# Kernel tuning notes

Measured on AMD Instinct MI355X. Metric: run time of the kernel, lower is better.

## Reference

```python
import jax, jax.numpy as jnp
import numpy as np

N, E, G = 20000, 320000, 32


def setup_inputs() -> dict:
    key = jax.random.key(0)
    ks = list(jax.random.split(key, 16))
    def nrm(i, shape, s):
        return jax.random.normal(ks[i], shape, jnp.float32) * s
    inp = {}
    inp['x'] = nrm(0, (N, 768), 1.0)
    inp['edge_index'] = jax.random.randint(ks[1], (2, E), 0, N)
    inp['batch'] = jnp.sort(jax.random.randint(ks[2], (N,), 0, G))
    # xavier-ish scales
    inp['proj_w'] = nrm(3, (768, 768), 0.036); inp['proj_b'] = jnp.zeros((768,), jnp.float32)
    inp['gat1_w'] = nrm(4, (768, 1024), 0.033)
    inp['att1_src'] = nrm(5, (4, 256), 0.06); inp['att1_dst'] = nrm(6, (4, 256), 0.06)
    inp['gat1_b'] = jnp.zeros((1024,), jnp.float32)
    inp['ln1_g'] = jnp.ones((1024,), jnp.float32); inp['ln1_b'] = jnp.zeros((1024,), jnp.float32)
    inp['gat2_w'] = nrm(7, (1024, 1024), 0.031)
    inp['att2_src'] = nrm(8, (4, 256), 0.06); inp['att2_dst'] = nrm(9, (4, 256), 0.06)
    inp['gat2_b'] = jnp.zeros((1024,), jnp.float32)
    inp['ln2_g'] = jnp.ones((1024,), jnp.float32); inp['ln2_b'] = jnp.zeros((1024,), jnp.float32)
    inp['gat3_w'] = nrm(10, (1024, 256), 0.04)
    inp['att3_src'] = nrm(11, (1, 256), 0.08); inp['att3_dst'] = nrm(12, (1, 256), 0.08)
    inp['gat3_b'] = jnp.zeros((256,), jnp.float32)
    inp['ln3_g'] = jnp.ones((256,), jnp.float32); inp['ln3_b'] = jnp.zeros((256,), jnp.float32)
    inp['cls1_w'] = nrm(13, (768, 128), 0.047); inp['cls1_b'] = jnp.zeros((128,), jnp.float32)
    inp['cls2_w'] = nrm(14, (128, 1), 0.12); inp['cls2_b'] = jnp.zeros((1,), jnp.float32)
    return inp


def layer_norm(x, g, b, eps=1e-5):
    mu = x.mean(-1, keepdims=True)
    v = ((x - mu) ** 2).mean(-1, keepdims=True)
    return (x - mu) * jax.lax.rsqrt(v + eps) * g + b


def gat_conv(x, src, dst, W, a_src, a_dst, bias, concat):
    # PyG GATConv (eval mode): linear -> per-head additive attention ->
    # segment softmax over incoming edges of each dst node -> scatter-sum.
    n = x.shape[0]
    H, C = a_src.shape
    h = (x @ W).reshape(n, H, C)                      # [N,H,C]
    e_s = (h * a_src[None]).sum(-1)                   # [N,H]
    e_d = (h * a_dst[None]).sum(-1)                   # [N,H]
    logits = jax.nn.leaky_relu(e_s[src] + e_d[dst], 0.2)   # [Etot,H]
    m = jax.ops.segment_max(logits, dst, num_segments=n)   # self-loops -> no empty segments
    ex = jnp.exp(logits - m[dst])
    den = jax.ops.segment_sum(ex, dst, num_segments=n)
    alpha = ex / (den[dst] + 1e-16)                   # [Etot,H]
    out = jax.ops.segment_sum(h[src] * alpha[:, :, None], dst, num_segments=n)  # [N,H,C]
    out = out.reshape(n, H * C) if concat else out.mean(axis=1)
    return out + bias


def reference(x, edge_index, batch, proj_w, proj_b,
              gat1_w, att1_src, att1_dst, gat1_b, ln1_g, ln1_b,
              gat2_w, att2_src, att2_dst, gat2_b, ln2_g, ln2_b,
              gat3_w, att3_src, att3_dst, gat3_b, ln3_g, ln3_b,
              cls1_w, cls1_b, cls2_w, cls2_b):
    n = x.shape[0]
    loop = jnp.arange(n)
    src = jnp.concatenate([edge_index[0], loop])  # GATConv adds self-loops
    dst = jnp.concatenate([edge_index[1], loop])
    h = jax.nn.elu(x @ proj_w + proj_b)
    x1 = jax.nn.elu(layer_norm(gat_conv(h, src, dst, gat1_w, att1_src, att1_dst, gat1_b, True), ln1_g, ln1_b))
    x2 = jax.nn.elu(layer_norm(gat_conv(x1, src, dst, gat2_w, att2_src, att2_dst, gat2_b, True), ln2_g, ln2_b)) + x1
    x3 = jax.nn.elu(layer_norm(gat_conv(x2, src, dst, gat3_w, att3_src, att3_dst, gat3_b, False), ln3_g, ln3_b))
    cnt = jax.ops.segment_sum(jnp.ones((n, 1), x3.dtype), batch, num_segments=G)
    s = jax.ops.segment_sum(x3, batch, num_segments=G)
    mean = s / jnp.maximum(cnt, 1.0)
    mx = jax.ops.segment_max(x3, batch, num_segments=G)
    pooled = jnp.concatenate([mean, mx, s], axis=1)   # [G, 3*256]
    out = jax.nn.relu(pooled @ cls1_w + cls1_b) @ cls2_w + cls2_b
    return out.reshape(-1)
```

## Files before the change

kernel.cpp:

```cpp
#include <hip/hip_runtime.h>
#include <math.h>

typedef float floatx4 __attribute__((ext_vector_type(4)));
typedef _Float16 f16x8 __attribute__((ext_vector_type(8)));
typedef _Float16 f16x4 __attribute__((ext_vector_type(4)));

__device__ __forceinline__ unsigned encf(float f) {
    unsigned u = __float_as_uint(f);
    return (u & 0x80000000u) ? ~u : (u | 0x80000000u);
}
__device__ __forceinline__ float decf(unsigned u) {
    u = (u & 0x80000000u) ? (u & 0x7FFFFFFFu) : ~u;
    return __uint_as_float(u);
}
__device__ __forceinline__ void glds16(const void* g, void* l) {
    __builtin_amdgcn_global_load_lds(
        (const __attribute__((address_space(1))) unsigned int*)g,
        (__attribute__((address_space(3))) unsigned int*)l, 16, 0, 0);
}

__global__ __launch_bounds__(256) void cvt_f16_kernel(
    const float* __restrict__ in, _Float16* __restrict__ out, size_t n4)
{
    size_t i = (size_t)blockIdx.x * 256 + threadIdx.x;
    if (i >= n4) return;
    float4 v = ((const float4*)in)[i];
    f16x4 o;
    o[0] = (_Float16)v.x; o[1] = (_Float16)v.y; o[2] = (_Float16)v.z; o[3] = (_Float16)v.w;
    ((f16x4*)out)[i] = o;
}

__global__ __launch_bounds__(256) void wt_kernel(
    const float* __restrict__ w, _Float16* __restrict__ wt, int K, int N)
{
    __shared__ float t[32][33];
    int bx = blockIdx.x * 32, by = blockIdx.y * 32;
    int tx = threadIdx.x & 31, ty = threadIdx.x >> 5;
    for (int r = ty; r < 32; r += 8)
        t[r][tx] = w[(size_t)(by + r) * N + bx + tx];
    __syncthreads();
    for (int r = ty; r < 32; r += 8)
        wt[(size_t)(bx + r) * K + by + tx] = (_Float16)t[tx][r];
}

__global__ __launch_bounds__(256) void gemm_f16(
    const _Float16* __restrict__ A, const _Float16* __restrict__ BT,
    const float* __restrict__ bias, _Float16* __restrict__ C,
    int M, int K, int N, int act)
{
    __shared__ _Float16 Al[2][128 * 32];
    __shared__ _Float16 Bl[2][128 * 32];
    int tid = threadIdx.x;
    int lane = tid & 63, wave = tid >> 6;
    int row0 = blockIdx.y * 128, col0 = blockIdx.x * 128;
    int wm = (wave >> 1) * 64, wn = (wave & 1) * 64;
    int l15 = lane & 15, quad = lane >> 4;

    int rg0 = wave * 2, rg1 = rg0 + 1;
    int srow0 = rg0 * 16 + (lane >> 2);
    int srow1 = rg1 * 16 + (lane >> 2);
    int scol = (lane & 3) * 8;
    int arow0 = row0 + srow0; if (arow0 > M - 1) arow0 = M - 1;
    int arow1 = row0 + srow1; if (arow1 > M - 1) arow1 = M - 1;
    const _Float16* gA0 = A + (size_t)arow0 * K + scol;
    const _Float16* gA1 = A + (size_t)arow1 * K + scol;
    const _Float16* gB0 = BT + (size_t)(col0 + srow0) * K + scol;
    const _Float16* gB1 = BT + (size_t)(col0 + srow1) * K + scol;

    floatx4 acc[4][4] = {};

    glds16(gA0, &Al[0][rg0 * 512]);
    glds16(gA1, &Al[0][rg1 * 512]);
    glds16(gB0, &Bl[0][rg0 * 512]);
    glds16(gB1, &Bl[0][rg1 * 512]);

    int nk = K >> 5;
    for (int it = 0; it < nk; it++) {
        int cur = it & 1, nxt = cur ^ 1;
        __syncthreads();
        if (it + 1 < nk) {
            int k1 = (it + 1) << 5;
            glds16(gA0 + k1, &Al[nxt][rg0 * 512]);
            glds16(gA1 + k1, &Al[nxt][rg1 * 512]);
            glds16(gB0 + k1, &Bl[nxt][rg0 * 512]);
            glds16(gB1 + k1, &Bl[nxt][rg1 * 512]);
        }
        f16x8 af[4], bfr[4];
        #pragma unroll
        for (int i = 0; i < 4; i++) {
            af[i]  = *(const f16x8*)&Al[cur][(wm + i * 16 + l15) * 32 + quad * 8];
            bfr[i] = *(const f16x8*)&Bl[cur][(wn + i * 16 + l15) * 32 + quad * 8];
        }
        #pragma unroll
        for (int i = 0; i < 4; i++)
            #pragma unroll
            for (int j = 0; j < 4; j++)
                acc[i][j] = __builtin_amdgcn_mfma_f32_16x16x32_f16(af[i], bfr[j], acc[i][j], 0, 0, 0);
    }

    #pragma unroll
    for (int i = 0; i < 4; i++) {
        #pragma unroll
        for (int v = 0; v < 4; v++) {
            int gr = row0 + wm + i * 16 + quad * 4 + v;
            if (gr >= M) continue;
            #pragma unroll
            for (int j = 0; j < 4; j++) {
                int gc = col0 + wn + j * 16 + l15;
                float val = acc[i][j][v];
                if (bias) val += bias[gc];
                if (act) val = val > 0.f ? val : (expf(val) - 1.f);
                C[(size_t)gr * N + gc] = (_Float16)val;
            }
        }
    }
}

__global__ __launch_bounds__(256) void attn_scores_kernel(
    const _Float16* __restrict__ h, const float* __restrict__ asrc, const float* __restrict__ adst,
    float* __restrict__ es, float* __restrict__ ed, int Nn, int H)
{
    int wid = (blockIdx.x * 256 + threadIdx.x) >> 6;
    int lane = threadIdx.x & 63;
    if (wid >= Nn * H) return;
    int node = wid / H, hh = wid % H;
    const _Float16* hp = h + (size_t)node * H * 256 + hh * 256 + lane * 4;
    f16x4 v = *(const f16x4*)hp;
    float ss = 0.f, sd = 0.f;
    #pragma unroll
    for (int j = 0; j < 4; j++) {
        float f = (float)v[j];
        ss = fmaf(f, asrc[hh * 256 + lane * 4 + j], ss);
        sd = fmaf(f, adst[hh * 256 + lane * 4 + j], sd);
    }
    #pragma unroll
    for (int o = 32; o; o >>= 1) { ss += __shfl_down(ss, o); sd += __shfl_down(sd, o); }
    if (lane == 0) { es[wid] = ss; ed[wid] = sd; }
}

__global__ __launch_bounds__(256) void csr_init(int* __restrict__ deg, int Nn) {
    int i = blockIdx.x * 256 + threadIdx.x;
    if (i < Nn) deg[i] = 1;
}
__global__ __launch_bounds__(256) void csr_count(const int* __restrict__ ei, int* __restrict__ deg, int E) {
    int i = blockIdx.x * 256 + threadIdx.x;
    if (i < E) atomicAdd(&deg[ei[E + i]], 1);
}
__global__ __launch_bounds__(256) void scan1(const int* __restrict__ deg, int* __restrict__ incl,
                                             int* __restrict__ bsums, int Nn) {
    __shared__ int sd[256];
    int idx = blockIdx.x * 256 + threadIdx.x;
    sd[threadIdx.x] = (idx < Nn) ? deg[idx] : 0;
    __syncthreads();
    for (int o = 1; o < 256; o <<= 1) {
        int x = (threadIdx.x >= (unsigned)o) ? sd[threadIdx.x - o] : 0;
        __syncthreads();
        sd[threadIdx.x] += x;
        __syncthreads();
    }
    if (idx < Nn) incl[idx] = sd[threadIdx.x];
    if (threadIdx.x == 255) bsums[blockIdx.x] = sd[255];
}
__global__ void scan2(int* __restrict__ bsums, int nb) {
    if (blockIdx.x == 0 && threadIdx.x == 0) {
        int run = 0;
        for (int i = 0; i < nb; i++) { int v = bsums[i]; bsums[i] = run; run += v; }
    }
}
__global__ __launch_bounds__(256) void scan3(const int* __restrict__ incl, const int* __restrict__ deg,
                                             const int* __restrict__ bsums, int* __restrict__ rowstart,
                                             int* __restrict__ cursor, int Nn) {
    int idx = blockIdx.x * 256 + threadIdx.x;
    if (idx >= Nn) return;
    int rs = incl[idx] - deg[idx] + bsums[blockIdx.x];
    rowstart[idx] = rs;
    cursor[idx] = rs;
}
__global__ __launch_bounds__(256) void csr_fill(const int* __restrict__ ei, int* __restrict__ cursor,
                                                int* __restrict__ csrc, int* __restrict__ cdst,
                                                int E, int Nn) {
    int i = blockIdx.x * 256 + threadIdx.x;
    if (i >= E + Nn) return;
    int s, d;
    if (i < E) { s = ei[i]; d = ei[E + i]; } else { s = d = i - E; }
    int pos = atomicAdd(&cursor[d], 1);
    csrc[pos] = s;
    cdst[pos] = d;
}

template<int H>
__global__ __launch_bounds__(256) void seg_mz(
    const int* __restrict__ rowstart, const int* __restrict__ deg,
    const int* __restrict__ csrc, const float* __restrict__ es,
    const float* __restrict__ ed, float2* __restrict__ mz, int Nn)
{
    int d = (blockIdx.x * 256 + threadIdx.x) >> 6;
    int lane = threadIdx.x & 63;
    if (d >= Nn) return;
    constexpr int S = 64 / H;
    int head = lane & (H - 1);
    int slot = lane / H;
    int st = rowstart[d], dg = deg[d];
    float edv = ed[d * H + head];
    float m = -1e30f;
    for (int j = slot; j < dg; j += S) {
        float l = es[csrc[st + j] * H + head] + edv;
        l = l > 0.f ? l : 0.2f * l;
        m = fmaxf(m, l);
    }
    #pragma unroll
    for (int o = H; o < 64; o <<= 1) m = fmaxf(m, __shfl_xor(m, o));
    float z = 0.f;
    for (int j = slot; j < dg; j += S) {
        float l = es[csrc[st + j] * H + head] + edv;
        l = l > 0.f ? l : 0.2f * l;
        z += expf(l - m);
    }
    #pragma unroll
    for (int o = H; o < 64; o <<= 1) z += __shfl_xor(z, o);
    if (lane < H) mz[d * H + lane] = make_float2(m, 1.f / (z + 1e-16f));
}

template<int H>
__global__ __launch_bounds__(256) void edge_alpha(
    const int* __restrict__ csrc, const int* __restrict__ cdst,
    const float* __restrict__ es, const float* __restrict__ ed,
    const float2* __restrict__ mz, float* __restrict__ wse, int Etot)
{
    int i = blockIdx.x * 256 + threadIdx.x;
    if (i >= Etot) return;
    int s = csrc[i], d = cdst[i];
    float a[H];
    #pragma unroll
    for (int hh = 0; hh < H; hh++) {
        float l = es[s * H + hh] + ed[d * H + hh];
        l = l > 0.f ? l : 0.2f * l;
        float2 mzv = mz[d * H + hh];
        a[hh] = expf(l - mzv.x) * mzv.y;
    }
    if constexpr (H == 4) {
        ((float4*)wse)[i] = make_float4(a[0], a[1], a[2], a[3]);
    } else {
        wse[i] = a[0];
    }
}

template<int H>
__global__ __launch_bounds__(64 * H) void gat_gather_ln(
    const int* __restrict__ rowstart, const int* __restrict__ deg,
    const int* __restrict__ csrc, const float* __restrict__ wse,
    const _Float16* __restrict__ h,
    const float* __restrict__ bias, const float* __restrict__ gam,
    const float* __restrict__ bet, const float* resid,
    float* xout, _Float16* xout16)
{
    constexpr int T = 64 * H;
    constexpr int NW = H;
    const int HC = T * 4;
    int d = blockIdx.x;
    int t = threadIdx.x;
    int lane = t & 63, wave = t >> 6;
    int head2 = t >> 6;
    int st = rowstart[d], dg = deg[d];
    const _Float16* hb = h + (size_t)t * 4;

    float a0 = 0.f, a1 = 0.f, a2 = 0.f, a3 = 0.f;
    int j = 0;
    for (; j + 2 <= dg; j += 2) {
        int s0 = csrc[st + j], s1 = csrc[st + j + 1];
        float w0 = wse[(size_t)(st + j) * H + head2];
        float w1 = wse[(size_t)(st + j + 1) * H + head2];
        f16x4 v0 = *(const f16x4*)(hb + (size_t)s0 * HC);
        f16x4 v1 = *(const f16x4*)(hb + (size_t)s1 * HC);
        a0 += w0 * (float)v0[0] + w1 * (float)v1[0];
        a1 += w0 * (float)v0[1] + w1 * (float)v1[1];
        a2 += w0 * (float)v0[2] + w1 * (float)v1[2];
        a3 += w0 * (float)v0[3] + w1 * (float)v1[3];
    }
    if (j < dg) {
        int s0 = csrc[st + j];
        float w0 = wse[(size_t)(st + j) * H + head2];
        f16x4 v0 = *(const f16x4*)(hb + (size_t)s0 * HC);
        a0 += w0 * (float)v0[0];
        a1 += w0 * (float)v0[1];
        a2 += w0 * (float)v0[2];
        a3 += w0 * (float)v0[3];
    }

    int c0 = t * 4;
    a0 += bias[c0]; a1 += bias[c0 + 1]; a2 += bias[c0 + 2]; a3 += bias[c0 + 3];

    __shared__ float sm[NW];
    float sum = a0 + a1 + a2 + a3;
    #pragma unroll
    for (int o = 32; o; o >>= 1) sum += __shfl_down(sum, o);
    if (lane == 0) sm[wave] = sum;
    __syncthreads();
    float tot = 0.f;
    #pragma unroll
    for (int w2 = 0; w2 < NW; w2++) tot += sm[w2];
    float mean = tot / (float)HC;
    float d0 = a0 - mean, d1 = a1 - mean, d2 = a2 - mean, d3 = a3 - mean;
    float sq = d0 * d0 + d1 * d1 + d2 * d2 + d3 * d3;
    #pragma unroll
    for (int o = 32; o; o >>= 1) sq += __shfl_down(sq, o);
    __syncthreads();
    if (lane == 0) sm[wave] = sq;
    __syncthreads();
    tot = 0.f;
    #pragma unroll
    for (int w2 = 0; w2 < NW; w2++) tot += sm[w2];
    float rstd = rsqrtf(tot / (float)HC + 1e-5f);

    float y0 = d0 * rstd * gam[c0]     + bet[c0];
    float y1 = d1 * rstd * gam[c0 + 1] + bet[c0 + 1];
    float y2 = d2 * rstd * gam[c0 + 2] + bet[c0 + 2];
    float y3 = d3 * rstd * gam[c0 + 3] + bet[c0 + 3];
    y0 = y0 > 0.f ? y0 : (expf(y0) - 1.f);
    y1 = y1 > 0.f ? y1 : (expf(y1) - 1.f);
    y2 = y2 > 0.f ? y2 : (expf(y2) - 1.f);
    y3 = y3 > 0.f ? y3 : (expf(y3) - 1.f);
    if (resid) {
        float4 r = ((const float4*)resid)[(size_t)d * T + t];
        y0 += r.x; y1 += r.y; y2 += r.z; y3 += r.w;
    }
    ((float4*)xout)[(size_t)d * T + t] = make_float4(y0, y1, y2, y3);
    if (xout16) {
        f16x4 o;
        o[0] = (_Float16)y0; o[1] = (_Float16)y1; o[2] = (_Float16)y2; o[3] = (_Float16)y3;
        ((f16x4*)xout16)[(size_t)d * T + t] = o;
    }
}

__global__ __launch_bounds__(256) void pool_kernel(
    const float* __restrict__ x3, const int* __restrict__ batch,
    float* __restrict__ ps, unsigned* __restrict__ pm, int* __restrict__ cnt, int Nn)
{
    int c = threadIdx.x;
    int n0 = blockIdx.x * 16;
    int end = n0 + 16; if (end > Nn) end = Nn;
    if (n0 >= Nn) return;
    int curg = batch[n0];
    float s = 0.f, m = -1e30f; int k = 0;
    for (int n = n0; n < end; n++) {
        int g = batch[n];
        if (g != curg) {
            atomicAdd(&ps[curg * 256 + c], s);
            atomicMax(&pm[curg * 256 + c], encf(m));
            if (c == 0) atomicAdd(&cnt[curg], k);
            s = 0.f; m = -1e30f; k = 0; curg = g;
        }
        float v = x3[(size_t)n * 256 + c];
        s += v; m = fmaxf(m, v); k++;
    }
    atomicAdd(&ps[curg * 256 + c], s);
    atomicMax(&pm[curg * 256 + c], encf(m));
    if (c == 0) atomicAdd(&cnt[curg], k);
}

__global__ __launch_bounds__(128) void classifier_kernel(
    const float* __restrict__ ps, const unsigned* __restrict__ pm, const int* __restrict__ cnt,
    const float* __restrict__ w1, const float* __restrict__ b1,
    const float* __restrict__ w2, const float* __restrict__ b2, float* __restrict__ out)
{
    int g = blockIdx.x;
    int tid = threadIdx.x;
    __shared__ float pooled[768];
    __shared__ float red[2];
    float c = (float)cnt[g];
    if (c < 1.f) c = 1.f;
    for (int i = tid; i < 256; i += 128) {
        float s = ps[g * 256 + i];
        pooled[i] = s / c;
        pooled[256 + i] = decf(pm[g * 256 + i]);
        pooled[512 + i] = s;
    }
    __syncthreads();
    float acc = b1[tid];
    for (int k = 0; k < 768; k++) acc = fmaf(pooled[k], w1[k * 128 + tid], acc);
    acc = fmaxf(acc, 0.f);
    float v = acc * w2[tid];
    #pragma unroll
    for (int o = 32; o; o >>= 1) v += __shfl_down(v, o);
    if ((tid & 63) == 0) red[tid >> 6] = v;
    __syncthreads();
    if (tid == 0) out[g] = red[0] + red[1] + b2[0];
}

extern "C" void kernel_launch(void* const* d_in, const int* in_sizes, int n_in,
                              void* d_out, int out_size, void* d_ws, size_t ws_size,
                              hipStream_t stream)
{
    const float* x      = (const float*)d_in[0];
    const int*   ei     = (const int*)d_in[1];
    const int*   batch  = (const int*)d_in[2];
    const float* proj_w = (const float*)d_in[3];
    const float* proj_b = (const float*)d_in[4];
    const float* gat1_w = (const float*)d_in[5];
    const float* att1_s = (const float*)d_in[6];
    const float* att1_d = (const float*)d_in[7];
    const float* gat1_b = (const float*)d_in[8];
    const float* ln1_g  = (const float*)d_in[9];
    const float* ln1_b  = (const float*)d_in[10];
    const float* gat2_w = (const float*)d_in[11];
    const float* att2_s = (const float*)d_in[12];
    const float* att2_d = (const float*)d_in[13];
    const float* gat2_b = (const float*)d_in[14];
    const float* ln2_g  = (const float*)d_in[15];
    const float* ln2_b  = (const float*)d_in[16];
    const float* gat3_w = (const float*)d_in[17];
    const float* att3_s = (const float*)d_in[18];
    const float* att3_d = (const float*)d_in[19];
    const float* gat3_b = (const float*)d_in[20];
    const float* ln3_g  = (const float*)d_in[21];
    const float* ln3_b  = (const float*)d_in[22];
    const float* cls1_w = (const float*)d_in[23];
    const float* cls1_b = (const float*)d_in[24];
    const float* cls2_w = (const float*)d_in[25];
    const float* cls2_b = (const float*)d_in[26];

    int Nn = in_sizes[0] / 768;
    int E  = in_sizes[1] / 2;
    int Gg = out_size;
    int Etot = E + Nn;
    int nb  = (Nn + 255) / 256;

    char* w = (char*)d_ws;
    size_t off = 0;
    auto alloc = [&](size_t bytes) -> char* {
        char* r = w + off;
        off += (bytes + 255) & ~(size_t)255;
        return r;
    };
    size_t NB16 = (size_t)Nn * 1024 * sizeof(_Float16);
    size_t NB32 = (size_t)Nn * 1024 * sizeof(float);
    _Float16* P = (_Float16*)alloc(NB16);
    _Float16* Q = (_Float16*)alloc(NB16);
    float*  X = (float*)alloc(NB32);
    _Float16* projT = (_Float16*)alloc((size_t)768 * 768 * 2);
    _Float16* g1T   = (_Float16*)alloc((size_t)1024 * 768 * 2);
    _Float16* g2T   = (_Float16*)alloc((size_t)1024 * 1024 * 2);
    _Float16* g3T   = (_Float16*)alloc((size_t)256 * 1024 * 2);
    float*    es    = (float*)alloc((size_t)Nn * 4 * 4);
    float*    ed_   = (float*)alloc((size_t)Nn * 4 * 4);
    float2*   mz    = (float2*)alloc((size_t)Nn * 4 * 8);
    int*      deg   = (int*)alloc((size_t)Nn * 4);
    int*      incl  = (int*)alloc((size_t)Nn * 4);
    int*      rowst = (int*)alloc((size_t)Nn * 4);
    int*      curs  = (int*)alloc((size_t)Nn * 4);
    int*      bsums = (int*)alloc((size_t)nb * 4);
    int*      csrc  = (int*)alloc((size_t)Etot * 4);
    int*      cdst  = (int*)alloc((size_t)Etot * 4);
    float*    wse   = (float*)alloc((size_t)Etot * 4 * 4);
    float*    ps    = (float*)alloc((size_t)Gg * 256 * 4);
    unsigned* pm    = (unsigned*)alloc((size_t)Gg * 256 * 4);
    int*      cnt   = (int*)alloc(256);

    dim3 blk(256);

    wt_kernel<<<dim3(768 / 32, 768 / 32), blk, 0, stream>>>(proj_w, projT, 768, 768);
    wt_kernel<<<dim3(1024 / 32, 768 / 32), blk, 0, stream>>>(gat1_w, g1T, 768, 1024);
    wt_kernel<<<dim3(1024 / 32, 1024 / 32), blk, 0, stream>>>(gat2_w, g2T, 1024, 1024);
    wt_kernel<<<dim3(256 / 32, 1024 / 32), blk, 0, stream>>>(gat3_w, g3T, 1024, 256);

    {
        size_t n4 = (size_t)Nn * 768 / 4;
        cvt_f16_kernel<<<dim3((unsigned)((n4 + 255) / 256)), blk, 0, stream>>>(x, P, n4);
    }

    csr_init<<<dim3(nb), blk, 0, stream>>>(deg, Nn);
    csr_count<<<dim3((E + 255) / 256), blk, 0, stream>>>(ei, deg, E);
    scan1<<<dim3(nb), blk, 0, stream>>>(deg, incl, bsums, Nn);
    scan2<<<dim3(1), dim3(64), 0, stream>>>(bsums, nb);
    scan3<<<dim3(nb), blk, 0, stream>>>(incl, deg, bsums, rowst, curs, Nn);
    csr_fill<<<dim3((Etot + 255) / 256), blk, 0, stream>>>(ei, curs, csrc, cdst, E, Nn);

    int mg = (Nn + 127) / 128;

    gemm_f16<<<dim3(768 / 128, mg), blk, 0, stream>>>(P, projT, proj_b, Q, Nn, 768, 768, 1);

    auto run_gat = [&](const _Float16* xin16, const _Float16* WT, const float* as_, const float* ad_,
                       const float* gb, const float* lg, const float* lb, const float* resid,
                       _Float16* hbuf, float* xout, _Float16* xout16,
                       int K, int H, int C) {
        int HC = H * C;
        gemm_f16<<<dim3(HC / 128, mg), blk, 0, stream>>>(xin16, WT, nullptr, hbuf, Nn, K, HC, 0);
        int nw = Nn * H;
        attn_scores_kernel<<<dim3((nw + 3) / 4), blk, 0, stream>>>(hbuf, as_, ad_, es, ed_, Nn, H);
        if (H == 4) {
            seg_mz<4><<<dim3((Nn + 3) / 4), blk, 0, stream>>>(rowst, deg, csrc, es, ed_, mz, Nn);
            edge_alpha<4><<<dim3((Etot + 255) / 256), blk, 0, stream>>>(csrc, cdst, es, ed_, mz, wse, Etot);
            gat_gather_ln<4><<<dim3(Nn), dim3(256), 0, stream>>>(rowst, deg, csrc, wse, hbuf,
                                                                 gb, lg, lb, resid, xout, xout16);
        } else {
            seg_mz<1><<<dim3((Nn + 3) / 4), blk, 0, stream>>>(rowst, deg, csrc, es, ed_, mz, Nn);
            edge_alpha<1><<<dim3((Etot + 255) / 256), blk, 0, stream>>>(csrc, cdst, es, ed_, mz, wse, Etot);
            gat_gather_ln<1><<<dim3(Nn), dim3(64), 0, stream>>>(rowst, deg, csrc, wse, hbuf,
                                                                gb, lg, lb, resid, xout, xout16);
        }
    };

    run_gat(Q, g1T, att1_s, att1_d, gat1_b, ln1_g, ln1_b, nullptr, P, X, Q, 768, 4, 256);
    run_gat(Q, g2T, att2_s, att2_d, gat2_b, ln2_g, ln2_b, X, P, X, Q, 1024, 4, 256);
    run_gat(Q, g3T, att3_s, att3_d, gat3_b, ln3_g, ln3_b, nullptr, P, X, nullptr, 1024, 1, 256);

    hipMemsetAsync(ps, 0, (size_t)Gg * 256 * 4, stream);
    hipMemsetAsync(pm, 0, (size_t)Gg * 256 * 4, stream);
    hipMemsetAsync(cnt, 0, (size_t)Gg * 4, stream);
    pool_kernel<<<dim3((Nn + 15) / 16), blk, 0, stream>>>(X, batch, ps, pm, cnt, Nn);
    classifier_kernel<<<dim3(Gg), dim3(128), 0, stream>>>(ps, pm, cnt, cls1_w, cls1_b, cls2_w, cls2_b, (float*)d_out);
}
```

Measured before the change: 814.2 us.

## Fuse edge softmax into segment kernel and widen gather to 8 channels per thread

The segment max/sum kernel now writes the per-edge logits, exponentials and normalized weights directly into the CSR-ordered weight buffer. This removes the separate edge_alpha kernel, the mz buffer and the cdst array, along with the repeated gathers of es/ed per edge. The 4-head gather+LayerNorm kernel now uses 128 threads, each handling 8 fp16 channels with 16-byte loads, which halves the thread count per node and cuts block-level sync. The trade-off is extra global read/write passes over wse inside the softmax kernel, and possibly lower occupancy or latency hiding in the gather.

```diff
diff --git a/kernel.cpp b/kernel.cpp
--- a/kernel.cpp
+++ b/kernel.cpp
@@ -4,6 +4,10 @@
 typedef float floatx4 __attribute__((ext_vector_type(4)));
 typedef _Float16 f16x8 __attribute__((ext_vector_type(8)));
 typedef _Float16 f16x4 __attribute__((ext_vector_type(4)));
+
+template<int N> struct f16vec_t;
+template<> struct f16vec_t<4> { typedef f16x4 type; };
+template<> struct f16vec_t<8> { typedef f16x8 type; };
 
 __device__ __forceinline__ unsigned encf(float f) {
     unsigned u = __float_as_uint(f);
@@ -177,22 +181,20 @@
     cursor[idx] = rs;
 }
 __global__ __launch_bounds__(256) void csr_fill(const int* __restrict__ ei, int* __restrict__ cursor,
-                                                int* __restrict__ csrc, int* __restrict__ cdst,
-                                                int E, int Nn) {
+                                                int* __restrict__ csrc, int E, int Nn) {
     int i = blockIdx.x * 256 + threadIdx.x;
     if (i >= E + Nn) return;
     int s, d;
     if (i < E) { s = ei[i]; d = ei[E + i]; } else { s = d = i - E; }
     int pos = atomicAdd(&cursor[d], 1);
     csrc[pos] = s;
-    cdst[pos] = d;
 }
 
 template<int H>
-__global__ __launch_bounds__(256) void seg_mz(
+__global__ __launch_bounds__(256) void seg_softmax(
     const int* __restrict__ rowstart, const int* __restrict__ deg,
     const int* __restrict__ csrc, const float* __restrict__ es,
-    const float* __restrict__ ed, float2* __restrict__ mz, int Nn)
+    const float* __restrict__ ed, float* __restrict__ wse, int Nn)
 {
     int d = (blockIdx.x * 256 + threadIdx.x) >> 6;
     int lane = threadIdx.x & 63;
@@ -206,47 +208,26 @@
     for (int j = slot; j < dg; j += S) {
         float l = es[csrc[st + j] * H + head] + edv;
         l = l > 0.f ? l : 0.2f * l;
+        wse[(size_t)(st + j) * H + head] = l;
         m = fmaxf(m, l);
     }
     #pragma unroll
     for (int o = H; o < 64; o <<= 1) m = fmaxf(m, __shfl_xor(m, o));
     float z = 0.f;
     for (int j = slot; j < dg; j += S) {
-        float l = es[csrc[st + j] * H + head] + edv;
-        l = l > 0.f ? l : 0.2f * l;
-        z += expf(l - m);
+        float e = expf(wse[(size_t)(st + j) * H + head] - m);
+        wse[(size_t)(st + j) * H + head] = e;
+        z += e;
     }
     #pragma unroll
     for (int o = H; o < 64; o <<= 1) z += __shfl_xor(z, o);
-    if (lane < H) mz[d * H + lane] = make_float2(m, 1.f / (z + 1e-16f));
+    float rz = 1.f / (z + 1e-16f);
+    for (int j = slot; j < dg; j += S)
+        wse[(size_t)(st + j) * H + head] *= rz;
 }
 
 template<int H>
-__global__ __launch_bounds__(256) void edge_alpha(
-    const int* __restrict__ csrc, const int* __restrict__ cdst,
-    const float* __restrict__ es, const float* __restrict__ ed,
-    const float2* __restrict__ mz, float* __restrict__ wse, int Etot)
-{
-    int i = blockIdx.x * 256 + threadIdx.x;
-    if (i >= Etot) return;
-    int s = csrc[i], d = cdst[i];
-    float a[H];
-    #pragma unroll
-    for (int hh = 0; hh < H; hh++) {
-        float l = es[s * H + hh] + ed[d * H + hh];
-        l = l > 0.f ? l : 0.2f * l;
-        float2 mzv = mz[d * H + hh];
-        a[hh] = expf(l - mzv.x) * mzv.y;
-    }
-    if constexpr (H == 4) {
-        ((float4*)wse)[i] = make_float4(a[0], a[1], a[2], a[3]);
-    } else {
-        wse[i] = a[0];
-    }
-}
-
-template<int H>
-__global__ __launch_bounds__(64 * H) void gat_gather_ln(
+__global__ __launch_bounds__(H == 4 ? 128 : 64) void gat_gather_ln(
     const int* __restrict__ rowstart, const int* __restrict__ deg,
     const int* __restrict__ csrc, const float* __restrict__ wse,
     const _Float16* __restrict__ h,
@@ -254,81 +235,101 @@
     const float* __restrict__ bet, const float* resid,
     float* xout, _Float16* xout16)
 {
-    constexpr int T = 64 * H;
-    constexpr int NW = H;
-    const int HC = T * 4;
+    constexpr int T = (H == 4) ? 128 : 64;
+    constexpr int CPT = (H == 4) ? 8 : 4;
+    constexpr int NW = T / 64;
+    constexpr int HC = H * 256;
+    typedef typename f16vec_t<CPT>::type hvec;
     int d = blockIdx.x;
     int t = threadIdx.x;
     int lane = t & 63, wave = t >> 6;
-    int head2 = t >> 6;
+    int ch0 = t * CPT;
+    int head2 = ch0 >> 8;
     int st = rowstart[d], dg = deg[d];
-    const _Float16* hb = h + (size_t)t * 4;
-
-    float a0 = 0.f, a1 = 0.f, a2 = 0.f, a3 = 0.f;
+    const _Float16* hb = h + ch0;
+
+    float acc[CPT];
+    #pragma unroll
+    for (int k = 0; k < CPT; k++) acc[k] = 0.f;
+
     int j = 0;
     for (; j + 2 <= dg; j += 2) {
         int s0 = csrc[st + j], s1 = csrc[st + j + 1];
         float w0 = wse[(size_t)(st + j) * H + head2];
         float w1 = wse[(size_t)(st + j + 1) * H + head2];
-        f16x4 v0 = *(const f16x4*)(hb + (size_t)s0 * HC);
-        f16x4 v1 = *(const f16x4*)(hb + (size_t)s1 * HC);
-        a0 += w0 * (float)v0[0] + w1 * (float)v1[0];
-        a1 += w0 * (float)v0[1] + w1 * (float)v1[1];
-        a2 += w0 * (float)v0[2] + w1 * (float)v1[2];
-        a3 += w0 * (float)v0[3] + w1 * (float)v1[3];
+        hvec v0 = *(const hvec*)(hb + (size_t)s0 * HC);
+        hvec v1 = *(const hvec*)(hb + (size_t)s1 * HC);
+        #pragma unroll
+        for (int k = 0; k < CPT; k++)
+            acc[k] += w0 * (float)v0[k] + w1 * (float)v1[k];
     }
     if (j < dg) {
         int s0 = csrc[st + j];
         float w0 = wse[(size_t)(st + j) * H + head2];
-        f16x4 v0 = *(const f16x4*)(hb + (size_t)s0 * HC);
-        a0 += w0 * (float)v0[0];
-        a1 += w0 * (float)v0[1];
-        a2 += w0 * (float)v0[2];
-        a3 += w0 * (float)v0[3];
-    }
-
-    int c0 = t * 4;
-    a0 += bias[c0]; a1 += bias[c0 + 1]; a2 += bias[c0 + 2]; a3 += bias[c0 + 3];
-
-    __shared__ float sm[NW];
-    float sum = a0 + a1 + a2 + a3;
+        hvec v0 = *(const hvec*)(hb + (size_t)s0 * HC);
+        #pragma unroll
+        for (int k = 0; k < CPT; k++) acc[k] += w0 * (float)v0[k];
+    }
+
+    #pragma unroll
+    for (int k = 0; k < CPT; k++) acc[k] += bias[ch0 + k];
+
+    __shared__ float sm[NW > 1 ? NW : 1];
+    float sum = 0.f;
+    #pragma unroll
+    for (int k = 0; k < CPT; k++) sum += acc[k];
     #pragma unroll
     for (int o = 32; o; o >>= 1) sum += __shfl_down(sum, o);
-    if (lane == 0) sm[wave] = sum;
-    __syncthreads();
-    float tot = 0.f;
-    #pragma unroll
-    for (int w2 = 0; w2 < NW; w2++) tot += sm[w2];
+    float tot;
+    if (NW > 1) {
+        if (lane == 0) sm[wave] = sum;
+        __syncthreads();
+        tot = 0.f;
+        #pragma unroll
+        for (int w2 = 0; w2 < NW; w2++) tot += sm[w2];
+    } else {
+        tot = __shfl(sum, 0);
+    }
     float mean = tot / (float)HC;
-    float d0 = a0 - mean, d1 = a1 - mean, d2 = a2 - mean, d3 = a3 - mean;
-    float sq = d0 * d0 + d1 * d1 + d2 * d2 + d3 * d3;
+    float sq = 0.f;
+    #pragma unroll
+    for (int k = 0; k < CPT; k++) { float dd = acc[k] - mean; sq = fmaf(dd, dd, sq); }
     #pragma unroll
     for (int o = 32; o; o >>= 1) sq += __shfl_down(sq, o);
-    __syncthreads();
-    if (lane == 0) sm[wave] = sq;
-    __syncthreads();
-    tot = 0.f;
-    #pragma unroll
-    for (int w2 = 0; w2 < NW; w2++) tot += sm[w2];
+    if (NW > 1) {
+        __syncthreads();
+        if (lane == 0) sm[wave] = sq;
+        __syncthreads();
+        tot = 0.f;
+        #pragma unroll
+        for (int w2 = 0; w2 < NW; w2++) tot += sm[w2];
+    } else {
+        tot = __shfl(sq, 0);
+    }
     float rstd = rsqrtf(tot / (float)HC + 1e-5f);
 
-    float y0 = d0 * rstd * gam[c0]     + bet[c0];
-    float y1 = d1 * rstd * gam[c0 + 1] + bet[c0 + 1];
-    float y2 = d2 * rstd * gam[c0 + 2] + bet[c0 + 2];
-    float y3 = d3 * rstd * gam[c0 + 3] + bet[c0 + 3];
-    y0 = y0 > 0.f ? y0 : (expf(y0) - 1.f);
-    y1 = y1 > 0.f ? y1 : (expf(y1) - 1.f);
-    y2 = y2 > 0.f ? y2 : (expf(y2) - 1.f);
-    y3 = y3 > 0.f ? y3 : (expf(y3) - 1.f);
+    float y[CPT];
+    #pragma unroll
+    for (int k = 0; k < CPT; k++) {
+        float v = (acc[k] - mean) * rstd * gam[ch0 + k] + bet[ch0 + k];
+        y[k] = v > 0.f ? v : (expf(v) - 1.f);
+    }
     if (resid) {
-        float4 r = ((const float4*)resid)[(size_t)d * T + t];
-        y0 += r.x; y1 += r.y; y2 += r.z; y3 += r.w;
-    }
-    ((float4*)xout)[(size_t)d * T + t] = make_float4(y0, y1, y2, y3);
+        #pragma unroll
+        for (int q = 0; q < CPT / 4; q++) {
+            float4 r = ((const float4*)resid)[(size_t)d * (HC / 4) + t * (CPT / 4) + q];
+            y[q * 4 + 0] += r.x; y[q * 4 + 1] += r.y; y[q * 4 + 2] += r.z; y[q * 4 + 3] += r.w;
+        }
+    }
+    #pragma unroll
+    for (int q = 0; q < CPT / 4; q++)
+        ((float4*)xout)[(size_t)d * (HC / 4) + t * (CPT / 4) + q] =
+            make_float4(y[q * 4 + 0], y[q * 4 + 1], y[q * 4 + 2], y[q * 4 + 3]);
     if (xout16) {
-        f16x4 o;
-        o[0] = (_Float16)y0; o[1] = (_Float16)y1; o[2] = (_Float16)y2; o[3] = (_Float16)y3;
-        ((f16x4*)xout16)[(size_t)d * T + t] = o;
+        hvec o;
+        #pragma unroll
+        for (int k = 0; k < CPT; k++) o[k] = (_Float16)y[k];
+        *(hvec*)(xout16 + (size_t)d * HC + ch0) = o;
     }
 }
 
@@ -443,14 +444,12 @@
     _Float16* g3T   = (_Float16*)alloc((size_t)256 * 1024 * 2);
     float*    es    = (float*)alloc((size_t)Nn * 4 * 4);
     float*    ed_   = (float*)alloc((size_t)Nn * 4 * 4);
-    float2*   mz    = (float2*)alloc((size_t)Nn * 4 * 8);
     int*      deg   = (int*)alloc((size_t)Nn * 4);
     int*      incl  = (int*)alloc((size_t)Nn * 4);
     int*      rowst = (int*)alloc((size_t)Nn * 4);
     int*      curs  = (int*)alloc((size_t)Nn * 4);
     int*      bsums = (int*)alloc((size_t)nb * 4);
     int*      csrc  = (int*)alloc((size_t)Etot * 4);
-    int*      cdst  = (int*)alloc((size_t)Etot * 4);
     float*    wse   = (float*)alloc((size_t)Etot * 4 * 4);
     float*    ps    = (float*)alloc((size_t)Gg * 256 * 4);
     unsigned* pm    = (unsigned*)alloc((size_t)Gg * 256 * 4);
@@ -473,7 +472,7 @@
     scan1<<<dim3(nb), blk, 0, stream>>>(deg, incl, bsums, Nn);
     scan2<<<dim3(1), dim3(64), 0, stream>>>(bsums, nb);
     scan3<<<dim3(nb), blk, 0, stream>>>(incl, deg, bsums, rowst, curs, Nn);
-    csr_fill<<<dim3((Etot + 255) / 256), blk, 0, stream>>>(ei, curs, csrc, cdst, E, Nn);
+    csr_fill<<<dim3((Etot + 255) / 256), blk, 0, stream>>>(ei, curs, csrc, E, Nn);
 
     int mg = (Nn + 127) / 128;
 
@@ -488,13 +487,11 @@
         int nw = Nn * H;
         attn_scores_kernel<<<dim3((nw + 3) / 4), blk, 0, stream>>>(hbuf, as_, ad_, es, ed_, Nn, H);
         if (H == 4) {
-            seg_mz<4><<<dim3((Nn + 3) / 4), blk, 0, stream>>>(rowst, deg, csrc, es, ed_, mz, Nn);
-            edge_alpha<4><<<dim3((Etot + 255) / 256), blk, 0, stream>>>(csrc, cdst, es, ed_, mz, wse, Etot);
-            gat_gather_ln<4><<<dim3(Nn), dim3(256), 0, stream>>>(rowst, deg, csrc, wse, hbuf,
+            seg_softmax<4><<<dim3((Nn + 3) / 4), blk, 0, stream>>>(rowst, deg, csrc, es, ed_, wse, Nn);
+            gat_gather_ln<4><<<dim3(Nn), dim3(128), 0, stream>>>(rowst, deg, csrc, wse, hbuf,
                                                                  gb, lg, lb, resid, xout, xout16);
         } else {
-            seg_mz<1><<<dim3((Nn + 3) / 4), blk, 0, stream>>>(rowst, deg, csrc, es, ed_, mz, Nn);
-            edge_alpha<1><<<dim3((Etot + 255) / 256), blk, 0, stream>>>(csrc, cdst, es, ed_, mz, wse, Etot);
+            seg_softmax<1><<<dim3((Nn + 3) / 4), blk, 0, stream>>>(rowst, deg, csrc, es, ed_, wse, Nn);
             gat_gather_ln<1><<<dim3(Nn), dim3(64), 0, stream>>>(rowst, deg, csrc, wse, hbuf,
                                                                 gb, lg, lb, resid, xout, xout16);
         }
```

Measured after the change: 807.1 us. No clear change (-0.9%).
